# Kernel optimization log

Measured on AMD Instinct MI355X. Metric: run time of the kernel, lower is better.

## Reference

```python
import jax, jax.numpy as jnp
import numpy as np

B, N, E, H = 16, 512, 256, 8
ALPHA = 0.2  # leaky relu negative slope


def setup_inputs() -> dict:
    key = jax.random.key(0)
    k1, k2, k3, k4, k5, k6 = jax.random.split(key, 6)
    x = jax.random.normal(k1, (B, N, E), dtype=jnp.float32)
    A = (jax.random.uniform(k2, (B, N, N)) < 0.3).astype(jnp.float32)
    s = 1.0 / np.sqrt(E)
    W = jax.random.uniform(k3, (E, E), minval=-s, maxval=s, dtype=jnp.float32)
    bW = jax.random.uniform(k4, (E,), minval=-s, maxval=s, dtype=jnp.float32)
    a = jax.random.uniform(k5, (E, 2 * H), minval=-s, maxval=s, dtype=jnp.float32)
    ba = jax.random.uniform(k6, (2 * H,), minval=-s, maxval=s, dtype=jnp.float32)
    return {"x": x, "A": A, "W": W, "bW": bW, "a": a, "ba": ba}


def reference(x, A, W, bW, a, ba):
    # Wh = W(x): [B, N, E]
    Wh = jnp.einsum("bne,ef->bnf", x, W) + bW
    # attention coefficients: a(Wh) -> [B, N, 2H] -> [B, H, N, 2]
    e12 = (jnp.einsum("bne,eh->bnh", Wh, a) + ba).reshape(B, N, H, 2).transpose(0, 2, 1, 3)
    e = e12[..., 0:1] + jnp.swapaxes(e12[..., 1:2], -2, -1)  # [B, H, N, N]
    # split heads: [B, H, N, D]
    Whh = Wh.reshape(B, N, H, E // H).transpose(0, 2, 1, 3)
    mask = A[:, None, :, :] > 0.5  # [B, H(bcast), N, N]
    neg = jnp.finfo(e.dtype).min
    score = jnp.where(mask, jax.nn.leaky_relu(e, ALPHA), neg)
    att = jax.nn.softmax(score, axis=-1)
    # rows with no neighbors: torch softmax(-inf row) -> nan -> nan_to_num -> 0
    has_nbr = jnp.any(mask, axis=-1, keepdims=True)
    att = jnp.where(has_nbr, att, 0.0)
    out = jnp.einsum("bhij,bhjd->bhid", att, Whh)  # [B, H, N, D]
    out = out.transpose(0, 2, 1, 3).reshape(B, N, E)
    # dropout is identity in eval/reference mode
    return jax.nn.relu(out)
```

## Files before the change

kernel.cpp:

```cpp
#include <hip/hip_runtime.h>
#include <math.h>

#define Bv 16
#define Nv 512
#define Ev 256
#define Hv 8
#define Dv 32
#define LOG2E 1.44269504088896340736f

typedef _Float16 half8 __attribute__((ext_vector_type(8)));
typedef _Float16 half4_t __attribute__((ext_vector_type(4)));
typedef __fp16 fp16x2 __attribute__((ext_vector_type(2)));
typedef float f32x4 __attribute__((ext_vector_type(4)));

__global__ __launch_bounds__(256) void fused_pre(const float* __restrict__ x,
                                                 const float* __restrict__ W,
                                                 const float* __restrict__ bW,
                                                 const float* __restrict__ aP,
                                                 const float* __restrict__ ba,
                                                 const float* __restrict__ A,
                                                 _Float16* __restrict__ WhT,
                                                 _Float16* __restrict__ WaT,
                                                 float* __restrict__ cba,
                                                 unsigned int* __restrict__ Abm) {
    __shared__ _Float16 Wp[64][264];
    __shared__ _Float16 xs[2][64][40];
    __shared__ _Float16 ldsTr[64][72];

    const int tid = threadIdx.x;
    const int blk = blockIdx.x;

    if (blk < 512) {
        const int m0 = (blk >> 2) * 64;
        const int n0 = (blk & 3) * 64;
        const int w = tid >> 6;
        const int lane = tid & 63;
        const int row = lane & 15;
        const int strip = lane >> 4;

        {
            const float* wrow = &W[(size_t)tid * Ev + n0];
            #pragma unroll
            for (int u = 0; u < 16; ++u) {
                float4 v = *(const float4*)&wrow[u * 4];
                Wp[u * 4 + 0][tid] = (_Float16)v.x;
                Wp[u * 4 + 1][tid] = (_Float16)v.y;
                Wp[u * 4 + 2][tid] = (_Float16)v.z;
                Wp[u * 4 + 3][tid] = (_Float16)v.w;
            }
        }

        const int sr = tid >> 2;
        const int skg = (tid & 3) * 8;
        const float* xrow = &x[(size_t)(m0 + sr) * Ev + skg];

        {
            float4 v0 = *(const float4*)xrow;
            float4 v1 = *(const float4*)(xrow + 4);
            half8 hv;
            hv[0] = (_Float16)v0.x; hv[1] = (_Float16)v0.y;
            hv[2] = (_Float16)v0.z; hv[3] = (_Float16)v0.w;
            hv[4] = (_Float16)v1.x; hv[5] = (_Float16)v1.y;
            hv[6] = (_Float16)v1.z; hv[7] = (_Float16)v1.w;
            *(half8*)&xs[0][sr][skg] = hv;
        }
        __syncthreads();

        f32x4 acc[4] = {{0.f, 0.f, 0.f, 0.f}, {0.f, 0.f, 0.f, 0.f},
                        {0.f, 0.f, 0.f, 0.f}, {0.f, 0.f, 0.f, 0.f}};
        int cur = 0;

        #pragma unroll
        for (int it = 0; it < 8; ++it) {
            float4 nv0, nv1;
            if (it < 7) {
                nv0 = *(const float4*)(xrow + (it + 1) * 32);
                nv1 = *(const float4*)(xrow + (it + 1) * 32 + 4);
            }

            half8 af = *(const half8*)&xs[cur][w * 16 + row][strip * 8];
            #pragma unroll
            for (int ns = 0; ns < 4; ++ns) {
                half8 bf = *(const half8*)&Wp[ns * 16 + row][it * 32 + strip * 8];
                acc[ns] = __builtin_amdgcn_mfma_f32_16x16x32_f16(af, bf, acc[ns], 0, 0, 0);
            }

            if (it < 7) {
                half8 hv;
                hv[0] = (_Float16)nv0.x; hv[1] = (_Float16)nv0.y;
                hv[2] = (_Float16)nv0.z; hv[3] = (_Float16)nv0.w;
                hv[4] = (_Float16)nv1.x; hv[5] = (_Float16)nv1.y;
                hv[6] = (_Float16)nv1.z; hv[7] = (_Float16)nv1.w;
                *(half8*)&xs[cur ^ 1][sr][skg] = hv;
                __syncthreads();
                cur ^= 1;
            }
        }

        #pragma unroll
        for (int ns = 0; ns < 4; ++ns) {
            const float bias = bW[n0 + ns * 16 + row];
            half4_t hv;
            hv[0] = (_Float16)(acc[ns][0] + bias);
            hv[1] = (_Float16)(acc[ns][1] + bias);
            hv[2] = (_Float16)(acc[ns][2] + bias);
            hv[3] = (_Float16)(acc[ns][3] + bias);
            *(half4_t*)&ldsTr[ns * 16 + row][w * 16 + strip * 4] = hv;
        }
        __syncthreads();

        {
            const int n = tid >> 2, jg = tid & 3;
            uint4 v0 = *(const uint4*)&ldsTr[n][jg * 16];
            uint4 v1 = *(const uint4*)&ldsTr[n][jg * 16 + 8];
            const int ng = n0 + n;
            const int h = ng >> 5, d = ng & 31;
            const int b = m0 >> 9, j0 = m0 & 511;
            _Float16* dst = &WhT[(((size_t)b * Hv + h) * Dv + d) * Nv + j0 + jg * 16];
            *(uint4*)dst = v0;
            *(uint4*)(dst + 8) = v1;
        }
    } else if (blk < 528) {
        const int e = (blk - 512) * 16 + (tid >> 4);
        const int c = tid & 15;
        float dot = 0.f;
        for (int k4 = 0; k4 < 64; ++k4) {
            float4 wv = *(const float4*)&W[(size_t)e * Ev + k4 * 4];
            dot += wv.x * aP[(k4 * 4 + 0) * 16 + c];
            dot += wv.y * aP[(k4 * 4 + 1) * 16 + c];
            dot += wv.z * aP[(k4 * 4 + 2) * 16 + c];
            dot += wv.w * aP[(k4 * 4 + 3) * 16 + c];
        }
        WaT[(size_t)c * Ev + e] = (_Float16)dot;
    } else if (blk == 528) {
        if (tid < 16) {
            float d = ba[tid];
            for (int k = 0; k < Ev; ++k) d += bW[k] * aP[k * 16 + tid];
            cba[tid] = d;
        }
    } else {
        const int ablk = blk - 529;
        const int w = tid >> 6, lane = tid & 63;
        const size_t base = (size_t)ablk * 2048 + w * 512;
        #pragma unroll
        for (int r = 0; r < 8; ++r) {
            const size_t f = base + r * 64 + lane;
            const bool pred = A[f] > 0.5f;
            unsigned long long m = __ballot(pred);
            if (lane == 0) *(unsigned long long*)&Abm[f >> 5] = m;
        }
    }
}

__global__ __launch_bounds__(64) void e12_mfma(const float* __restrict__ x,
                                               const _Float16* __restrict__ WaT,
                                               const float* __restrict__ cba,
                                               float* __restrict__ e1,
                                               float* __restrict__ e2) {
    const int lane = threadIdx.x;
    const int m0 = blockIdx.x * 16;
    const int l15 = lane & 15;
    const int strip = lane >> 4;

    const float* xr = &x[(size_t)(m0 + l15) * Ev + strip * 8];
    const _Float16* wr = &WaT[(size_t)l15 * Ev + strip * 8];

    f32x4 acc = {0.f, 0.f, 0.f, 0.f};
    #pragma unroll
    for (int kt = 0; kt < 8; ++kt) {
        float4 a0 = *(const float4*)&xr[kt * 32];
        float4 a1 = *(const float4*)&xr[kt * 32 + 4];
        fp16x2 h0 = __builtin_amdgcn_cvt_pkrtz(a0.x, a0.y);
        fp16x2 h1 = __builtin_amdgcn_cvt_pkrtz(a0.z, a0.w);
        fp16x2 h2 = __builtin_amdgcn_cvt_pkrtz(a1.x, a1.y);
        fp16x2 h3 = __builtin_amdgcn_cvt_pkrtz(a1.z, a1.w);
        uint4 U;
        U.x = __builtin_bit_cast(unsigned int, h0);
        U.y = __builtin_bit_cast(unsigned int, h1);
        U.z = __builtin_bit_cast(unsigned int, h2);
        U.w = __builtin_bit_cast(unsigned int, h3);
        half8 af = __builtin_bit_cast(half8, U);
        half8 bf = *(const half8*)&wr[kt * 32];
        acc = __builtin_amdgcn_mfma_f32_16x16x32_f16(af, bf, acc, 0, 0, 0);
    }

    const int c = l15;
    const float cb = cba[c];
    const int h = c >> 1;
    float* dst = (c & 1) ? e2 : e1;
    #pragma unroll
    for (int e = 0; e < 4; ++e) {
        const int m = m0 + strip * 4 + e;
        const int b = m >> 9, i = m & 511;
        dst[(((b << 3) + h) << 9) + i] = acc[e] + cb;
    }
}

__global__ __launch_bounds__(256) void attn_kernel(const unsigned int* __restrict__ Abm,
                                                   const _Float16* __restrict__ WhT,
                                                   const float* __restrict__ e1g,
                                                   const float* __restrict__ e2g,
                                                   float* __restrict__ out) {
    __shared__ _Float16 whT[Dv * Nv];
    __shared__ float E2pS[Nv];
    __shared__ float E2nS[Nv];

    const int tid = threadIdx.x;
    const int i0 = blockIdx.x * 128;
    const int h = blockIdx.y;
    const int b = blockIdx.z;
    const int bh = (b << 3) + h;

    const _Float16* src = WhT + (size_t)bh * (Dv * Nv);
    #pragma unroll
    for (int u = 0; u < 8; ++u) {
        int f = tid + u * 256;
        int d = f >> 6, bq = f & 63;
        uint4 v = *(const uint4*)(src + d * Nv + bq * 8);
        *(uint4*)&whT[d * Nv + ((bq ^ (d & 7)) * 8)] = v;
    }
    {
        float ea = e2g[(bh << 9) + tid] * LOG2E;
        E2pS[tid] = __builtin_amdgcn_exp2f(ea);
        E2nS[tid] = __builtin_amdgcn_exp2f(0.2f * ea);
        float eb = e2g[(bh << 9) + tid + 256] * LOG2E;
        E2pS[tid + 256] = __builtin_amdgcn_exp2f(eb);
        E2nS[tid + 256] = __builtin_amdgcn_exp2f(0.2f * eb);
    }
    __syncthreads();

    const int w = tid >> 6;
    const int lane = tid & 63;
    const int row = lane & 15;
    const int strip = lane >> 4;
    const int iA = i0 + (w << 5) + row;
    const int iB = iA + 16;

    const float e1A = e1g[(bh << 9) + iA] * LOG2E;
    const float e1B = e1g[(bh << 9) + iB] * LOG2E;
    const float E1pA = __builtin_amdgcn_exp2f(e1A);
    const float E1nA = __builtin_amdgcn_exp2f(0.2f * e1A);
    const float E1pB = __builtin_amdgcn_exp2f(e1B);
    const float E1nB = __builtin_amdgcn_exp2f(0.2f * e1B);

    const uint4* bpA = (const uint4*)&Abm[((size_t)b * Nv + iA) << 4];
    const uint4 mA0 = bpA[0], mA1 = bpA[1], mA2 = bpA[2], mA3 = bpA[3];
    const uint4* bpB = (const uint4*)&Abm[((size_t)b * Nv + iB) << 4];
    const uint4 mB0 = bpB[0], mB1 = bpB[1], mB2 = bpB[2], mB3 = bpB[3];

    const int sh = strip << 3;
    const int d0 = lane & 15;
    const int sw = d0 & 7;
    const _Float16* brow0 = &whT[d0 * Nv];
    const _Float16* brow1 = &whT[(16 + d0) * Nv];

    f32x4 accA0 = {0.f, 0.f, 0.f, 0.f}, accA1 = accA0;
    f32x4 accB0 = accA0, accB1 = accA0;
    float denA = 0.f, denB = 0.f;

    #pragma unroll
    for (int t = 0; t < 16; ++t) {
        const uint4 mqA = (t >> 2) == 0 ? mA0 : (t >> 2) == 1 ? mA1 : (t >> 2) == 2 ? mA2 : mA3;
        const uint4 mqB = (t >> 2) == 0 ? mB0 : (t >> 2) == 1 ? mB1 : (t >> 2) == 2 ? mB2 : mB3;
        const unsigned int dwA = (t & 3) == 0 ? mqA.x : (t & 3) == 1 ? mqA.y : (t & 3) == 2 ? mqA.z : mqA.w;
        const unsigned int dwB = (t & 3) == 0 ? mqB.x : (t & 3) == 1 ? mqB.y : (t & 3) == 2 ? mqB.z : mqB.w;
        const unsigned int byA = (dwA >> sh) & 0xFFu;
        const unsigned int byB = (dwB >> sh) & 0xFFu;

        const float4 p0 = *(const float4*)&E2pS[t * 32 + sh];
        const float4 p1 = *(const float4*)&E2pS[t * 32 + sh + 4];
        const float4 n0 = *(const float4*)&E2nS[t * 32 + sh];
        const float4 n1 = *(const float4*)&E2nS[t * 32 + sh + 4];

        const float qA0 = (byA & 1u)   ? fmaxf(E1pA * p0.x, E1nA * n0.x) : 0.f;
        const float qA1 = (byA & 2u)   ? fmaxf(E1pA * p0.y, E1nA * n0.y) : 0.f;
        const float qA2 = (byA & 4u)   ? fmaxf(E1pA * p0.z, E1nA * n0.z) : 0.f;
        const float qA3 = (byA & 8u)   ? fmaxf(E1pA * p0.w, E1nA * n0.w) : 0.f;
        const float qA4 = (byA & 16u)  ? fmaxf(E1pA * p1.x, E1nA * n1.x) : 0.f;
        const float qA5 = (byA & 32u)  ? fmaxf(E1pA * p1.y, E1nA * n1.y) : 0.f;
        const float qA6 = (byA & 64u)  ? fmaxf(E1pA * p1.z, E1nA * n1.z) : 0.f;
        const float qA7 = (byA & 128u) ? fmaxf(E1pA * p1.w, E1nA * n1.w) : 0.f;
        const float qB0 = (byB & 1u)   ? fmaxf(E1pB * p0.x, E1nB * n0.x) : 0.f;
        const float qB1 = (byB & 2u)   ? fmaxf(E1pB * p0.y, E1nB * n0.y) : 0.f;
        const float qB2 = (byB & 4u)   ? fmaxf(E1pB * p0.z, E1nB * n0.z) : 0.f;
        const float qB3 = (byB & 8u)   ? fmaxf(E1pB * p0.w, E1nB * n0.w) : 0.f;
        const float qB4 = (byB & 16u)  ? fmaxf(E1pB * p1.x, E1nB * n1.x) : 0.f;
        const float qB5 = (byB & 32u)  ? fmaxf(E1pB * p1.y, E1nB * n1.y) : 0.f;
        const float qB6 = (byB & 64u)  ? fmaxf(E1pB * p1.z, E1nB * n1.z) : 0.f;
        const float qB7 = (byB & 128u) ? fmaxf(E1pB * p1.w, E1nB * n1.w) : 0.f;

        denA += ((qA0 + qA1) + (qA2 + qA3)) + ((qA4 + qA5) + (qA6 + qA7));
        denB += ((qB0 + qB1) + (qB2 + qB3)) + ((qB4 + qB5) + (qB6 + qB7));

        fp16x2 a01 = __builtin_amdgcn_cvt_pkrtz(qA0, qA1);
        fp16x2 a23 = __builtin_amdgcn_cvt_pkrtz(qA2, qA3);
        fp16x2 a45 = __builtin_amdgcn_cvt_pkrtz(qA4, qA5);
        fp16x2 a67 = __builtin_amdgcn_cvt_pkrtz(qA6, qA7);
        fp16x2 b01 = __builtin_amdgcn_cvt_pkrtz(qB0, qB1);
        fp16x2 b23 = __builtin_amdgcn_cvt_pkrtz(qB2, qB3);
        fp16x2 b45 = __builtin_amdgcn_cvt_pkrtz(qB4, qB5);
        fp16x2 b67 = __builtin_amdgcn_cvt_pkrtz(qB6, qB7);

        uint4 UA, UB;
        UA.x = __builtin_bit_cast(unsigned int, a01);
        UA.y = __builtin_bit_cast(unsigned int, a23);
        UA.z = __builtin_bit_cast(unsigned int, a45);
        UA.w = __builtin_bit_cast(unsigned int, a67);
        UB.x = __builtin_bit_cast(unsigned int, b01);
        UB.y = __builtin_bit_cast(unsigned int, b23);
        UB.z = __builtin_bit_cast(unsigned int, b45);
        UB.w = __builtin_bit_cast(unsigned int, b67);
        half8 afA = __builtin_bit_cast(half8, UA);
        half8 afB = __builtin_bit_cast(half8, UB);

        const int bq = ((t << 2) + strip) ^ sw;
        half8 b0 = *(const half8*)(brow0 + bq * 8);
        half8 b1 = *(const half8*)(brow1 + bq * 8);
        accA0 = __builtin_amdgcn_mfma_f32_16x16x32_f16(afA, b0, accA0, 0, 0, 0);
        accA1 = __builtin_amdgcn_mfma_f32_16x16x32_f16(afA, b1, accA1, 0, 0, 0);
        accB0 = __builtin_amdgcn_mfma_f32_16x16x32_f16(afB, b0, accB0, 0, 0, 0);
        accB1 = __builtin_amdgcn_mfma_f32_16x16x32_f16(afB, b1, accB1, 0, 0, 0);
    }

    denA += __shfl_xor(denA, 16);
    denA += __shfl_xor(denA, 32);
    denB += __shfl_xor(denB, 16);
    denB += __shfl_xor(denB, 32);

    #pragma unroll
    for (int e = 0; e < 4; ++e) {
        const float dnA = __shfl(denA, (strip << 2) + e);
        const float rvA = (dnA > 0.f) ? (1.f / dnA) : 0.f;
        const int orA = i0 + (w << 5) + (strip << 2) + e;
        float* opA = &out[((size_t)b * Nv + orA) * Ev + (h << 5)];
        opA[d0] = fmaxf(accA0[e] * rvA, 0.f);
        opA[16 + d0] = fmaxf(accA1[e] * rvA, 0.f);

        const float dnB = __shfl(denB, (strip << 2) + e);
        const float rvB = (dnB > 0.f) ? (1.f / dnB) : 0.f;
        const int orB = orA + 16;
        float* opB = &out[((size_t)b * Nv + orB) * Ev + (h << 5)];
        opB[d0] = fmaxf(accB0[e] * rvB, 0.f);
        opB[16 + d0] = fmaxf(accB1[e] * rvB, 0.f);
    }
}

extern "C" void kernel_launch(void* const* d_in, const int* in_sizes, int n_in,
                              void* d_out, int out_size, void* d_ws, size_t ws_size,
                              hipStream_t stream) {
    const float* x  = (const float*)d_in[0];
    const float* A  = (const float*)d_in[1];
    const float* W  = (const float*)d_in[2];
    const float* bW = (const float*)d_in[3];
    const float* a  = (const float*)d_in[4];
    const float* ba = (const float*)d_in[5];
    float* out = (float*)d_out;

    char* ws = (char*)d_ws;
    _Float16*     WaT = (_Float16*)(ws);
    float*        cba = (float*)(ws + 16384);
    float*        e1  = (float*)(ws + 32768);
    float*        e2  = (float*)(ws + 294912);
    unsigned int* Abm = (unsigned int*)(ws + 557056);
    _Float16*     WhT = (_Float16*)(ws + 1572864);

    fused_pre<<<2577, 256, 0, stream>>>(x, W, bW, a, ba, A, WhT, WaT, cba, Abm);
    e12_mfma<<<Bv * Nv / 16, 64, 0, stream>>>(x, WaT, cba, e1, e2);
    attn_kernel<<<dim3(Nv / 128, Hv, Bv), 256, 0, stream>>>(Abm, WhT, e1, e2, out);
}
```

Measured before the change: 41.88 us.

## Fuse attention-logit projection into the Wh GEMM epilogue and drop e12 kernel

Removes the separate e12 MFMA kernel and the W·a precompute blocks. Each Wh GEMM tile now multiplies its fp16 Wh tile by the matching slice of `a` and writes partial e1/e2 sums per 64-column quarter. The attention kernel adds the four partials plus the bias. The attention kernel is also reshaped to 128-thread blocks covering 64 rows, which doubles the grid and the number of per-block WhT loads into LDS. The goal is to save one kernel launch and a pass over x, at the cost of extra partial-sum reads and redundant staging in attention.

```diff
diff --git a/kernel.cpp b/kernel.cpp
--- a/kernel.cpp
+++ b/kernel.cpp
@@ -17,15 +17,13 @@
                                                  const float* __restrict__ W,
                                                  const float* __restrict__ bW,
                                                  const float* __restrict__ aP,
-                                                 const float* __restrict__ ba,
                                                  const float* __restrict__ A,
                                                  _Float16* __restrict__ WhT,
-                                                 _Float16* __restrict__ WaT,
-                                                 float* __restrict__ cba,
+                                                 float* __restrict__ e12part,
                                                  unsigned int* __restrict__ Abm) {
     __shared__ _Float16 Wp[64][264];
     __shared__ _Float16 xs[2][64][40];
-    __shared__ _Float16 ldsTr[64][72];
+    __shared__ _Float16 ldsTr[64][68];
 
     const int tid = threadIdx.x;
     const int blk = blockIdx.x;
@@ -120,26 +118,30 @@
             *(uint4*)dst = v0;
             *(uint4*)(dst + 8) = v1;
         }
-    } else if (blk < 528) {
-        const int e = (blk - 512) * 16 + (tid >> 4);
-        const int c = tid & 15;
-        float dot = 0.f;
-        for (int k4 = 0; k4 < 64; ++k4) {
-            float4 wv = *(const float4*)&W[(size_t)e * Ev + k4 * 4];
-            dot += wv.x * aP[(k4 * 4 + 0) * 16 + c];
-            dot += wv.y * aP[(k4 * 4 + 1) * 16 + c];
-            dot += wv.z * aP[(k4 * 4 + 2) * 16 + c];
-            dot += wv.w * aP[(k4 * 4 + 3) * 16 + c];
-        }
-        WaT[(size_t)c * Ev + e] = (_Float16)dot;
-    } else if (blk == 528) {
-        if (tid < 16) {
-            float d = ba[tid];
-            for (int k = 0; k < Ev; ++k) d += bW[k] * aP[k * 16 + tid];
-            cba[tid] = d;
+
+        {
+            const int nq = n0 >> 6;
+            const int b = m0 >> 9, j0 = m0 & 511;
+            const int jA = lane & 15;
+            f32x4 eacc = {0.f, 0.f, 0.f, 0.f};
+            #pragma unroll
+            for (int kh = 0; kh < 2; ++kh) {
+                half8 af, bf;
+                #pragma unroll
+                for (int e = 0; e < 8; ++e) {
+                    const int kf = kh * 32 + strip * 8 + e;
+                    af[e] = ldsTr[kf][w * 16 + jA];
+                    bf[e] = (_Float16)aP[(n0 + kf) * 16 + jA];
+                }
+                eacc = __builtin_amdgcn_mfma_f32_16x16x32_f16(af, bf, eacc, 0, 0, 0);
+            }
+            const int c = jA;
+            float* dst = &e12part[(((size_t)(nq * 16 + c)) * Bv + b) * Nv +
+                                  j0 + w * 16 + strip * 4];
+            *(f32x4*)dst = eacc;
         }
     } else {
-        const int ablk = blk - 529;
+        const int ablk = blk - 512;
         const int w = tid >> 6, lane = tid & 63;
         const size_t base = (size_t)ablk * 2048 + w * 512;
         #pragma unroll
@@ -152,80 +154,50 @@
     }
 }
 
-__global__ __launch_bounds__(64) void e12_mfma(const float* __restrict__ x,
-                                               const _Float16* __restrict__ WaT,
-                                               const float* __restrict__ cba,
-                                               float* __restrict__ e1,
-                                               float* __restrict__ e2) {
-    const int lane = threadIdx.x;
-    const int m0 = blockIdx.x * 16;
-    const int l15 = lane & 15;
-    const int strip = lane >> 4;
-
-    const float* xr = &x[(size_t)(m0 + l15) * Ev + strip * 8];
-    const _Float16* wr = &WaT[(size_t)l15 * Ev + strip * 8];
-
-    f32x4 acc = {0.f, 0.f, 0.f, 0.f};
-    #pragma unroll
-    for (int kt = 0; kt < 8; ++kt) {
-        float4 a0 = *(const float4*)&xr[kt * 32];
-        float4 a1 = *(const float4*)&xr[kt * 32 + 4];
-        fp16x2 h0 = __builtin_amdgcn_cvt_pkrtz(a0.x, a0.y);
-        fp16x2 h1 = __builtin_amdgcn_cvt_pkrtz(a0.z, a0.w);
-        fp16x2 h2 = __builtin_amdgcn_cvt_pkrtz(a1.x, a1.y);
-        fp16x2 h3 = __builtin_amdgcn_cvt_pkrtz(a1.z, a1.w);
-        uint4 U;
-        U.x = __builtin_bit_cast(unsigned int, h0);
-        U.y = __builtin_bit_cast(unsigned int, h1);
-        U.z = __builtin_bit_cast(unsigned int, h2);
-        U.w = __builtin_bit_cast(unsigned int, h3);
-        half8 af = __builtin_bit_cast(half8, U);
-        half8 bf = *(const half8*)&wr[kt * 32];
-        acc = __builtin_amdgcn_mfma_f32_16x16x32_f16(af, bf, acc, 0, 0, 0);
-    }
-
-    const int c = l15;
-    const float cb = cba[c];
-    const int h = c >> 1;
-    float* dst = (c & 1) ? e2 : e1;
-    #pragma unroll
-    for (int e = 0; e < 4; ++e) {
-        const int m = m0 + strip * 4 + e;
-        const int b = m >> 9, i = m & 511;
-        dst[(((b << 3) + h) << 9) + i] = acc[e] + cb;
-    }
-}
-
-__global__ __launch_bounds__(256) void attn_kernel(const unsigned int* __restrict__ Abm,
+__global__ __launch_bounds__(128) void attn_kernel(const unsigned int* __restrict__ Abm,
                                                    const _Float16* __restrict__ WhT,
-                                                   const float* __restrict__ e1g,
-                                                   const float* __restrict__ e2g,
+                                                   const float* __restrict__ e12part,
+                                                   const float* __restrict__ baP,
                                                    float* __restrict__ out) {
     __shared__ _Float16 whT[Dv * Nv];
     __shared__ float E2pS[Nv];
     __shared__ float E2nS[Nv];
 
     const int tid = threadIdx.x;
-    const int i0 = blockIdx.x * 128;
+    const int i0 = blockIdx.x * 64;
     const int h = blockIdx.y;
     const int b = blockIdx.z;
     const int bh = (b << 3) + h;
 
     const _Float16* src = WhT + (size_t)bh * (Dv * Nv);
     #pragma unroll
-    for (int u = 0; u < 8; ++u) {
-        int f = tid + u * 256;
+    for (int u = 0; u < 16; ++u) {
+        int f = tid + u * 128;
         int d = f >> 6, bq = f & 63;
         uint4 v = *(const uint4*)(src + d * Nv + bq * 8);
         *(uint4*)&whT[d * Nv + ((bq ^ (d & 7)) * 8)] = v;
     }
     {
-        float ea = e2g[(bh << 9) + tid] * LOG2E;
-        E2pS[tid] = __builtin_amdgcn_exp2f(ea);
-        E2nS[tid] = __builtin_amdgcn_exp2f(0.2f * ea);
-        float eb = e2g[(bh << 9) + tid + 256] * LOG2E;
-        E2pS[tid + 256] = __builtin_amdgcn_exp2f(eb);
-        E2nS[tid + 256] = __builtin_amdgcn_exp2f(0.2f * eb);
+        const float ba2 = baP[2 * h + 1];
+        const int c2 = 2 * h + 1;
+        float4 s = {0.f, 0.f, 0.f, 0.f};
+        #pragma unroll
+        for (int nq = 0; nq < 4; ++nq) {
+            float4 v = *(const float4*)&e12part[(((size_t)(nq * 16 + c2)) * Bv + b) * Nv + tid * 4];
+            s.x += v.x; s.y += v.y; s.z += v.z; s.w += v.w;
+        }
+        const float v0 = (s.x + ba2) * LOG2E;
+        const float v1 = (s.y + ba2) * LOG2E;
+        const float v2 = (s.z + ba2) * LOG2E;
+        const float v3 = (s.w + ba2) * LOG2E;
+        E2pS[tid * 4 + 0] = __builtin_amdgcn_exp2f(v0);
+        E2pS[tid * 4 + 1] = __builtin_amdgcn_exp2f(v1);
+        E2pS[tid * 4 + 2] = __builtin_amdgcn_exp2f(v2);
+        E2pS[tid * 4 + 3] = __builtin_amdgcn_exp2f(v3);
+        E2nS[tid * 4 + 0] = __builtin_amdgcn_exp2f(0.2f * v0);
+        E2nS[tid * 4 + 1] = __builtin_amdgcn_exp2f(0.2f * v1);
+        E2nS[tid * 4 + 2] = __builtin_amdgcn_exp2f(0.2f * v2);
+        E2nS[tid * 4 + 3] = __builtin_amdgcn_exp2f(0.2f * v3);
     }
     __syncthreads();
 
@@ -236,8 +208,16 @@
     const int iA = i0 + (w << 5) + row;
     const int iB = iA + 16;
 
-    const float e1A = e1g[(bh << 9) + iA] * LOG2E;
-    const float e1B = e1g[(bh << 9) + iB] * LOG2E;
+    const int c1 = 2 * h;
+    float e1Araw = baP[c1], e1Braw = baP[c1];
+    #pragma unroll
+    for (int nq = 0; nq < 4; ++nq) {
+        const float* p = &e12part[(((size_t)(nq * 16 + c1)) * Bv + b) * Nv];
+        e1Araw += p[iA];
+        e1Braw += p[iB];
+    }
+    const float e1A = e1Araw * LOG2E;
+    const float e1B = e1Braw * LOG2E;
     const float E1pA = __builtin_amdgcn_exp2f(e1A);
     const float E1nA = __builtin_amdgcn_exp2f(0.2f * e1A);
     const float E1pB = __builtin_amdgcn_exp2f(e1B);
@@ -357,14 +337,10 @@
     float* out = (float*)d_out;
 
     char* ws = (char*)d_ws;
-    _Float16*     WaT = (_Float16*)(ws);
-    float*        cba = (float*)(ws + 16384);
-    float*        e1  = (float*)(ws + 32768);
-    float*        e2  = (float*)(ws + 294912);
-    unsigned int* Abm = (unsigned int*)(ws + 557056);
-    _Float16*     WhT = (_Float16*)(ws + 1572864);
-
-    fused_pre<<<2577, 256, 0, stream>>>(x, W, bW, a, ba, A, WhT, WaT, cba, Abm);
-    e12_mfma<<<Bv * Nv / 16, 64, 0, stream>>>(x, WaT, cba, e1, e2);
-    attn_kernel<<<dim3(Nv / 128, Hv, Bv), 256, 0, stream>>>(Abm, WhT, e1, e2, out);
+    float*        e12part = (float*)(ws);
+    unsigned int* Abm     = (unsigned int*)(ws + 2097152);
+    _Float16*     WhT     = (_Float16*)(ws + 2621440);
+
+    fused_pre<<<2560, 256, 0, stream>>>(x, W, bW, a, A, WhT, e12part, Abm);
+    attn_kernel<<<dim3(8, Hv, Bv), 128, 0, stream>>>(Abm, WhT, e12part, ba, out);
 }
```

New measurement: 40.14 us. 4.2% less time.
